# Performance work log

Hardware: AMD Instinct MI355X
Metric: run time of the kernel (lower is better)

The kernel has to match this reference:

```python
import jax, jax.numpy as jnp
import numpy as np

EMB = 128  # embsize
WORD = 128  # word_size
ITERS = 2


def _agg(embeds, neibors):
    # embeds: [B, N, D], neibors: [B, N, K] indices into node axis N (per batch)
    # mean-pool gathered neighbor embeddings -> [B, N, D]
    gathered = jax.vmap(lambda e, idx: e[idx])(embeds, neibors)  # [B, N, K, D]
    return gathered.mean(axis=2)


def setup_inputs() -> dict:
    key = jax.random.key(0)
    ks = jax.random.split(key, 9)
    B, N, K = 64, 512, 16
    word_embs = jax.random.normal(ks[0], (B, N, WORD), dtype=jnp.float32)
    lib_embs = jax.random.normal(ks[1], (B, N, WORD), dtype=jnp.float32)
    neibors = jax.random.randint(ks[2], (B, N, K), 0, N)
    neibors_lib = jax.random.randint(ks[3], (B, N, K), 0, N)
    mask = jax.random.uniform(ks[4], (B, N), dtype=jnp.float32)
    # xavier-uniform style params
    def xav(k, shape):
        bound = float(np.sqrt(6.0 / (shape[0] + shape[1])))
        return jax.random.uniform(k, shape, dtype=jnp.float32, minval=-bound, maxval=bound)
    weight = xav(ks[5], (WORD, EMB))
    weight2 = xav(ks[6], (EMB, EMB))
    enc_w1 = xav(ks[7], (WORD, EMB))
    enc_w2 = xav(ks[8], (EMB, EMB))
    return {"word_embs": word_embs, "neibors": neibors, "lib_embs": lib_embs,
            "neibors_lib": neibors_lib, "mask": mask, "weight": weight,
            "weight2": weight2, "enc_w1": enc_w1, "enc_w2": enc_w2}


def reference(word_embs, neibors, lib_embs, neibors_lib, mask, weight, weight2, enc_w1, enc_w2):
    B, N, _ = word_embs.shape
    # lib aggregation is loop-invariant (lib_embs fixed); same math as in-loop recompute
    agg_lib = jnp.einsum('bnw,we->bne', _agg(lib_embs, neibors_lib), weight)  # [B, N, EMB]
    word_proj = jnp.einsum('bnw,we->bne', word_embs, enc_w1)  # loop-invariant
    last_embed = jnp.zeros((B, N, EMB), dtype=jnp.float32)
    for _ in range(ITERS):
        agg_func = _agg(last_embed, neibors)  # [B, N, EMB]
        last_embed = jnp.tanh(word_proj + jnp.einsum('bne,ef->bnf', agg_func, enc_w2) + agg_lib)
    # masked sum over nodes, then final linear
    pooled = (last_embed * mask[:, :, None]).sum(axis=1)  # [B, EMB]
    return pooled @ weight2
```

## Files before the change

### kernel.cpp

```cpp
#include <hip/hip_runtime.h>
#include <hip/hip_bf16.h>

#define B_   64
#define N_   512
#define K_   16
#define D_   128
#define NPB  16
#define G1   ((B_*N_)/NPB)

typedef float f32x4  __attribute__((ext_vector_type(4)));
typedef short bf16x8 __attribute__((ext_vector_type(8)));

static __device__ __forceinline__ short f2bf(float x) {
    union { float f; unsigned u; } v; v.f = x;
    unsigned r = v.u + 0x7fffu + ((v.u >> 16) & 1u);
    return (short)(r >> 16);
}
static __device__ __forceinline__ float bfbits2f(unsigned hi_bits) {
    return __uint_as_float(hi_bits);
}
static __device__ __forceinline__ float bf2f(short h) {
    return __uint_as_float(((unsigned)(unsigned short)h) << 16);
}
static __device__ __forceinline__ float fast_tanh(float x) {
    float e = __expf(2.f * x);
    return 1.f - 2.f * __builtin_amdgcn_rcpf(e + 1.f);
}

__global__ __launch_bounds__(256) void prep(const float* __restrict__ lib,
                                            const float* __restrict__ enc1,
                                            const float* __restrict__ wgt,
                                            const float* __restrict__ enc2,
                                            short* __restrict__ libh,
                                            short* __restrict__ Bp1,
                                            short* __restrict__ Bp2,
                                            float* __restrict__ out) {
    const int blk = blockIdx.x;
    if (blk < 1024) {
        const size_t g = ((size_t)blk * 256 + threadIdx.x) * 16;
        short o16[16];
#pragma unroll
        for (int q = 0; q < 4; ++q) {
            float4 v = *(const float4*)&lib[g + q * 4];
            o16[q * 4 + 0] = f2bf(v.x); o16[q * 4 + 1] = f2bf(v.y);
            o16[q * 4 + 2] = f2bf(v.z); o16[q * 4 + 3] = f2bf(v.w);
        }
        *(int4*)&libh[g]     = *(int4*)o16;
        *(int4*)&libh[g + 8] = *(int4*)(o16 + 8);
        return;
    }
    int tid = (blk - 1024) * 256 + threadIdx.x;
    out[tid] = 0.f;
    short o8[8];
    if (tid < 4096) {
        int l = tid & 63, nt = (tid >> 6) & 7, ks = tid >> 9;
        int k0 = ks * 32 + (l >> 4) * 8;
        int col = nt * 16 + (l & 15);
#pragma unroll
        for (int j = 0; j < 8; ++j) {
            int r = k0 + j;
            float v = (r < 128) ? enc1[r * 128 + col] : wgt[(r - 128) * 128 + col];
            o8[j] = f2bf(v);
        }
        *(int4*)&Bp1[(size_t)tid * 8] = *(int4*)o8;
    } else if (tid < 6144) {
        int t2 = tid - 4096;
        int l = t2 & 63, nt = (t2 >> 6) & 7, ks = t2 >> 9;
        int k0 = ks * 32 + (l >> 4) * 8;
        int col = nt * 16 + (l & 15);
#pragma unroll
        for (int j = 0; j < 8; ++j) o8[j] = f2bf(enc2[(k0 + j) * 128 + col]);
        *(int4*)&Bp2[(size_t)t2 * 8] = *(int4*)o8;
    }
}

static __device__ __forceinline__ int swz_blk() {
    const int hw = blockIdx.x;
    return ((hw & 7) << 8) + (hw >> 3);
}

#define LDA1 264
__global__ __launch_bounds__(256) void gemm1(const float* __restrict__ word,
                                             const int* __restrict__ nbrL,
                                             const short* __restrict__ libh,
                                             const short* __restrict__ Bp1,
                                             short* __restrict__ baseh,
                                             short* __restrict__ t1) {
    __shared__ short sA[NPB * LDA1];
    __shared__ int sIdx[NPB * 16];
    const int tid = threadIdx.x;
    const int blk = swz_blk();
    const int b = blk >> 5;
    const int node0 = blk * NPB;

    if (tid < 64) *(int4*)&sIdx[tid * 4] = *(const int4*)&nbrL[(size_t)node0 * 16 + tid * 4];
    __syncthreads();

    const int w = tid >> 6, l = tid & 63;
    const int rh = l >> 5, c4 = l & 31;
    const short* libB = libh + (size_t)b * N_ * D_;

#pragma unroll
    for (int p = 0; p < 2; ++p) {
        const int row = 4 * w + 2 * p + rh;
        const int gid = node0 + row;
        float4 wv = *(const float4*)&word[(size_t)gid * D_ + c4 * 4];
        short4 ws; ws.x = f2bf(wv.x); ws.y = f2bf(wv.y); ws.z = f2bf(wv.z); ws.w = f2bf(wv.w);
        *(short4*)&sA[row * LDA1 + c4 * 4] = ws;
        int idxr[16];
#pragma unroll
        for (int k = 0; k < 16; ++k) idxr[k] = sIdx[row * 16 + k];
        float s0 = 0.f, s1 = 0.f, s2 = 0.f, s3 = 0.f;
#pragma unroll
        for (int k = 0; k < 16; ++k) {
            uint2 u = *(const uint2*)&libB[(size_t)idxr[k] * D_ + c4 * 4];
            s0 += bfbits2f(u.x << 16); s1 += bfbits2f(u.x & 0xffff0000u);
            s2 += bfbits2f(u.y << 16); s3 += bfbits2f(u.y & 0xffff0000u);
        }
        short4 as; as.x = f2bf(s0 * 0.0625f); as.y = f2bf(s1 * 0.0625f);
        as.z = f2bf(s2 * 0.0625f); as.w = f2bf(s3 * 0.0625f);
        *(short4*)&sA[row * LDA1 + 128 + c4 * 4] = as;
    }
    __syncthreads();

    f32x4 acc[2];
    acc[0] = (f32x4)0.f; acc[1] = (f32x4)0.f;

    const int arow = l & 15;
#pragma unroll
    for (int ks = 0; ks < 8; ++ks) {
        bf16x8 a = *(const bf16x8*)&sA[arow * LDA1 + ks * 32 + (l >> 4) * 8];
#pragma unroll
        for (int j = 0; j < 2; ++j) {
            const int nt = 2 * w + j;
            bf16x8 bb = *(const bf16x8*)&Bp1[((size_t)(ks * 8 + nt) * 64 + l) * 8];
            acc[j] = __builtin_amdgcn_mfma_f32_16x16x32_bf16(a, bb, acc[j], 0, 0, 0);
        }
    }

    const int r0 = (l >> 4) * 4;
    const int cl = l & 15;
#pragma unroll
    for (int j = 0; j < 2; ++j) {
        const int col = (2 * w + j) * 16 + cl;
#pragma unroll
        for (int r = 0; r < 4; ++r) {
            size_t o = (size_t)(node0 + r0 + r) * D_ + col;
            float v = acc[j][r];
            baseh[o] = f2bf(v);
            t1[o]    = f2bf(fast_tanh(v));
        }
    }
}

#define LDA2 136
__global__ __launch_bounds__(256) void gemm2(const short* __restrict__ t1,
                                             const int* __restrict__ nbr,
                                             const short* __restrict__ Bp2,
                                             const short* __restrict__ baseh,
                                             const float* __restrict__ mask,
                                             const float* __restrict__ w2,
                                             float* __restrict__ out) {
    __shared__ short sA[NPB * LDA2];
    __shared__ int sIdx[NPB * 16];
    __shared__ float pred[128];
    __shared__ float smask[NPB];
    const int tid = threadIdx.x;
    const int blk = swz_blk();
    const int b = blk >> 5;
    const int node0 = blk * NPB;

    if (tid < 64) *(int4*)&sIdx[tid * 4] = *(const int4*)&nbr[(size_t)node0 * 16 + tid * 4];
    if (tid >= 64 && tid < 64 + NPB) smask[tid - 64] = mask[node0 + tid - 64];
    __syncthreads();

    const int w = tid >> 6, l = tid & 63;
    const int rh = l >> 5, c4 = l & 31;
    const short* t1B = t1 + (size_t)b * N_ * D_;

#pragma unroll
    for (int p = 0; p < 2; ++p) {
        const int row = 4 * w + 2 * p + rh;
        int idxr[16];
#pragma unroll
        for (int k = 0; k < 16; ++k) idxr[k] = sIdx[row * 16 + k];
        float s0 = 0.f, s1 = 0.f, s2 = 0.f, s3 = 0.f;
#pragma unroll
        for (int k = 0; k < 16; ++k) {
            uint2 u = *(const uint2*)&t1B[(size_t)idxr[k] * D_ + c4 * 4];
            s0 += bfbits2f(u.x << 16); s1 += bfbits2f(u.x & 0xffff0000u);
            s2 += bfbits2f(u.y << 16); s3 += bfbits2f(u.y & 0xffff0000u);
        }
        short4 as; as.x = f2bf(s0 * 0.0625f); as.y = f2bf(s1 * 0.0625f);
        as.z = f2bf(s2 * 0.0625f); as.w = f2bf(s3 * 0.0625f);
        *(short4*)&sA[row * LDA2 + c4 * 4] = as;
    }
    __syncthreads();

    f32x4 acc[2];
    acc[0] = (f32x4)0.f; acc[1] = (f32x4)0.f;

    const int arow = l & 15;
#pragma unroll
    for (int ks = 0; ks < 4; ++ks) {
        bf16x8 a = *(const bf16x8*)&sA[arow * LDA2 + ks * 32 + (l >> 4) * 8];
#pragma unroll
        for (int j = 0; j < 2; ++j) {
            const int nt = 2 * w + j;
            bf16x8 bb = *(const bf16x8*)&Bp2[((size_t)(ks * 8 + nt) * 64 + l) * 8];
            acc[j] = __builtin_amdgcn_mfma_f32_16x16x32_bf16(a, bb, acc[j], 0, 0, 0);
        }
    }

    const int r0 = (l >> 4) * 4;
    const int cl = l & 15;
#pragma unroll
    for (int j = 0; j < 2; ++j) {
        const int col = (2 * w + j) * 16 + cl;
        float s = 0.f;
#pragma unroll
        for (int r = 0; r < 4; ++r) {
            size_t o = (size_t)(node0 + r0 + r) * D_ + col;
            float v = fast_tanh(bf2f(baseh[o]) + acc[j][r]);
            s += v * smask[r0 + r];
        }
        s += __shfl_xor(s, 16);
        s += __shfl_xor(s, 32);
        if (l < 16) pred[col] = s;
    }
    __syncthreads();
    if (tid < 128) {
        float a2 = 0.f;
#pragma unroll 4
        for (int f = 0; f < 128; ++f) a2 += pred[f] * w2[f * 128 + tid];
        atomicAdd(&out[b * 128 + tid], a2);
    }
}

extern "C" void kernel_launch(void* const* d_in, const int* in_sizes, int n_in,
                              void* d_out, int out_size, void* d_ws, size_t ws_size,
                              hipStream_t stream) {
    const float* word_embs   = (const float*)d_in[0];
    const int*   neibors     = (const int*)d_in[1];
    const float* lib_embs    = (const float*)d_in[2];
    const int*   neibors_lib = (const int*)d_in[3];
    const float* mask        = (const float*)d_in[4];
    const float* weight      = (const float*)d_in[5];
    const float* weight2     = (const float*)d_in[6];
    const float* enc_w1      = (const float*)d_in[7];
    const float* enc_w2      = (const float*)d_in[8];
    float* out = (float*)d_out;

    char* ws = (char*)d_ws;
    short* baseh = (short*)(ws);
    short* t1    = (short*)(ws + (1u << 23));
    short* libh  = (short*)(ws + (2u << 23));
    short* Bp1   = (short*)(ws + (3u << 23));
    short* Bp2   = (short*)(ws + (3u << 23) + 65536);

    prep<<<1056, 256, 0, stream>>>(lib_embs, enc_w1, weight, enc_w2, libh, Bp1, Bp2, out);
    gemm1<<<G1, 256, 0, stream>>>(word_embs, neibors_lib, libh, Bp1, baseh, t1);
    gemm2<<<G1, 256, 0, stream>>>(t1, neibors, Bp2, baseh, mask, weight2, out);
}
```

Measured before the change: 49.59 us.

## Switch intermediates to fp16 with packed-add gathers and folded mean scale

Converts all stored intermediates and MFMA operands from bf16 to fp16. This lets neighbor gathers accumulate with v_pk_add_f16 directly on packed data instead of unpacking to fp32. The 1/16 mean factor is folded into the weight matrices, and each thread now gathers full 16-byte rows (int4) instead of 8-byte pieces. This cuts ALU work and instruction count in the gather phase, at the cost of fp16 range and accumulation precision when summing 16 neighbors.

```diff
diff --git a/kernel.cpp b/kernel.cpp
--- a/kernel.cpp
+++ b/kernel.cpp
@@ -3,28 +3,29 @@
 
 #define B_   64
 #define N_   512
-#define K_   16
 #define D_   128
 #define NPB  16
 #define G1   ((B_*N_)/NPB)
 
 typedef float f32x4  __attribute__((ext_vector_type(4)));
-typedef short bf16x8 __attribute__((ext_vector_type(8)));
-
-static __device__ __forceinline__ short f2bf(float x) {
-    union { float f; unsigned u; } v; v.f = x;
-    unsigned r = v.u + 0x7fffu + ((v.u >> 16) & 1u);
-    return (short)(r >> 16);
-}
-static __device__ __forceinline__ float bfbits2f(unsigned hi_bits) {
-    return __uint_as_float(hi_bits);
-}
-static __device__ __forceinline__ float bf2f(short h) {
-    return __uint_as_float(((unsigned)(unsigned short)h) << 16);
+typedef _Float16 f16x8 __attribute__((ext_vector_type(8)));
+
+static __device__ __forceinline__ unsigned pkrtz(float x, float y) {
+    return __builtin_bit_cast(unsigned, __builtin_amdgcn_cvt_pkrtz(x, y));
+}
+static __device__ __forceinline__ short f2h(float x) {
+    _Float16 h = (_Float16)x;
+    return __builtin_bit_cast(short, h);
+}
+static __device__ __forceinline__ float h2f(short s) {
+    return (float)__builtin_bit_cast(_Float16, s);
 }
 static __device__ __forceinline__ float fast_tanh(float x) {
     float e = __expf(2.f * x);
     return 1.f - 2.f * __builtin_amdgcn_rcpf(e + 1.f);
+}
+static __device__ __forceinline__ void pk_add16(unsigned& acc, unsigned v) {
+    asm("v_pk_add_f16 %0, %1, %0" : "+v"(acc) : "v"(v));
 }
 
 __global__ __launch_bounds__(256) void prep(const float* __restrict__ lib,
@@ -38,15 +39,15 @@
     const int blk = blockIdx.x;
     if (blk < 1024) {
         const size_t g = ((size_t)blk * 256 + threadIdx.x) * 16;
-        short o16[16];
+        unsigned o[8];
 #pragma unroll
         for (int q = 0; q < 4; ++q) {
             float4 v = *(const float4*)&lib[g + q * 4];
-            o16[q * 4 + 0] = f2bf(v.x); o16[q * 4 + 1] = f2bf(v.y);
-            o16[q * 4 + 2] = f2bf(v.z); o16[q * 4 + 3] = f2bf(v.w);
-        }
-        *(int4*)&libh[g]     = *(int4*)o16;
-        *(int4*)&libh[g + 8] = *(int4*)(o16 + 8);
+            o[q * 2]     = pkrtz(v.x, v.y);
+            o[q * 2 + 1] = pkrtz(v.z, v.w);
+        }
+        *(int4*)&libh[g]     = *(int4*)o;
+        *(int4*)&libh[g + 8] = *(int4*)(o + 4);
         return;
     }
     int tid = (blk - 1024) * 256 + threadIdx.x;
@@ -59,8 +60,8 @@
 #pragma unroll
         for (int j = 0; j < 8; ++j) {
             int r = k0 + j;
-            float v = (r < 128) ? enc1[r * 128 + col] : wgt[(r - 128) * 128 + col];
-            o8[j] = f2bf(v);
+            float v = (r < 128) ? enc1[r * 128 + col] : wgt[(r - 128) * 128 + col] * 0.0625f;
+            o8[j] = f2h(v);
         }
         *(int4*)&Bp1[(size_t)tid * 8] = *(int4*)o8;
     } else if (tid < 6144) {
@@ -69,7 +70,7 @@
         int k0 = ks * 32 + (l >> 4) * 8;
         int col = nt * 16 + (l & 15);
 #pragma unroll
-        for (int j = 0; j < 8; ++j) o8[j] = f2bf(enc2[(k0 + j) * 128 + col]);
+        for (int j = 0; j < 8; ++j) o8[j] = f2h(enc2[(k0 + j) * 128 + col] * 0.0625f);
         *(int4*)&Bp2[(size_t)t2 * 8] = *(int4*)o8;
     }
 }
@@ -80,6 +81,8 @@
 }
 
 #define LDA1 264
+#define LDA2 136
+
 __global__ __launch_bounds__(256) void gemm1(const float* __restrict__ word,
                                              const int* __restrict__ nbrL,
                                              const short* __restrict__ libh,
@@ -96,45 +99,49 @@
     if (tid < 64) *(int4*)&sIdx[tid * 4] = *(const int4*)&nbrL[(size_t)node0 * 16 + tid * 4];
     __syncthreads();
 
+    const int row = tid >> 4;
+    const int lg  = tid & 15;
+
+    {
+        const float* wr = word + (size_t)(node0 + row) * D_ + lg * 8;
+        float4 v0 = *(const float4*)&wr[0];
+        float4 v1 = *(const float4*)&wr[4];
+        unsigned o[4] = { pkrtz(v0.x, v0.y), pkrtz(v0.z, v0.w),
+                          pkrtz(v1.x, v1.y), pkrtz(v1.z, v1.w) };
+        *(int4*)&sA[row * LDA1 + lg * 8] = *(int4*)o;
+    }
+
+    {
+        int idxr[16];
+#pragma unroll
+        for (int q = 0; q < 4; ++q) *(int4*)&idxr[q * 4] = *(const int4*)&sIdx[row * 16 + q * 4];
+        const char* libB = (const char*)libh + (size_t)b * N_ * D_ * 2 + lg * 16;
+        unsigned a0 = 0, a1 = 0, a2 = 0, a3 = 0;
+#pragma unroll
+        for (int nb = 0; nb < 16; ++nb) {
+            int4 d = *(const int4*)(libB + ((unsigned)idxr[nb] << 8));
+            pk_add16(a0, (unsigned)d.x);
+            pk_add16(a1, (unsigned)d.y);
+            pk_add16(a2, (unsigned)d.z);
+            pk_add16(a3, (unsigned)d.w);
+        }
+        unsigned o[4] = { a0, a1, a2, a3 };
+        *(int4*)&sA[row * LDA1 + 128 + lg * 8] = *(int4*)o;
+    }
+    __syncthreads();
+
     const int w = tid >> 6, l = tid & 63;
-    const int rh = l >> 5, c4 = l & 31;
-    const short* libB = libh + (size_t)b * N_ * D_;
-
-#pragma unroll
-    for (int p = 0; p < 2; ++p) {
-        const int row = 4 * w + 2 * p + rh;
-        const int gid = node0 + row;
-        float4 wv = *(const float4*)&word[(size_t)gid * D_ + c4 * 4];
-        short4 ws; ws.x = f2bf(wv.x); ws.y = f2bf(wv.y); ws.z = f2bf(wv.z); ws.w = f2bf(wv.w);
-        *(short4*)&sA[row * LDA1 + c4 * 4] = ws;
-        int idxr[16];
-#pragma unroll
-        for (int k = 0; k < 16; ++k) idxr[k] = sIdx[row * 16 + k];
-        float s0 = 0.f, s1 = 0.f, s2 = 0.f, s3 = 0.f;
-#pragma unroll
-        for (int k = 0; k < 16; ++k) {
-            uint2 u = *(const uint2*)&libB[(size_t)idxr[k] * D_ + c4 * 4];
-            s0 += bfbits2f(u.x << 16); s1 += bfbits2f(u.x & 0xffff0000u);
-            s2 += bfbits2f(u.y << 16); s3 += bfbits2f(u.y & 0xffff0000u);
-        }
-        short4 as; as.x = f2bf(s0 * 0.0625f); as.y = f2bf(s1 * 0.0625f);
-        as.z = f2bf(s2 * 0.0625f); as.w = f2bf(s3 * 0.0625f);
-        *(short4*)&sA[row * LDA1 + 128 + c4 * 4] = as;
-    }
-    __syncthreads();
-
     f32x4 acc[2];
     acc[0] = (f32x4)0.f; acc[1] = (f32x4)0.f;
-
     const int arow = l & 15;
 #pragma unroll
     for (int ks = 0; ks < 8; ++ks) {
-        bf16x8 a = *(const bf16x8*)&sA[arow * LDA1 + ks * 32 + (l >> 4) * 8];
+        f16x8 a = *(const f16x8*)&sA[arow * LDA1 + ks * 32 + (l >> 4) * 8];
 #pragma unroll
         for (int j = 0; j < 2; ++j) {
             const int nt = 2 * w + j;
-            bf16x8 bb = *(const bf16x8*)&Bp1[((size_t)(ks * 8 + nt) * 64 + l) * 8];
-            acc[j] = __builtin_amdgcn_mfma_f32_16x16x32_bf16(a, bb, acc[j], 0, 0, 0);
+            f16x8 bb = *(const f16x8*)&Bp1[((size_t)(ks * 8 + nt) * 64 + l) * 8];
+            acc[j] = __builtin_amdgcn_mfma_f32_16x16x32_f16(a, bb, acc[j], 0, 0, 0);
         }
     }
 
@@ -147,13 +154,12 @@
         for (int r = 0; r < 4; ++r) {
             size_t o = (size_t)(node0 + r0 + r) * D_ + col;
             float v = acc[j][r];
-            baseh[o] = f2bf(v);
-            t1[o]    = f2bf(fast_tanh(v));
-        }
-    }
-}
-
-#define LDA2 136
+            baseh[o] = f2h(v);
+            t1[o]    = f2h(fast_tanh(v));
+        }
+    }
+}
+
 __global__ __launch_bounds__(256) void gemm2(const short* __restrict__ t1,
                                              const int* __restrict__ nbr,
                                              const short* __restrict__ Bp2,
@@ -174,41 +180,39 @@
     if (tid >= 64 && tid < 64 + NPB) smask[tid - 64] = mask[node0 + tid - 64];
     __syncthreads();
 
+    const int row = tid >> 4;
+    const int lg  = tid & 15;
+    {
+        int idxr[16];
+#pragma unroll
+        for (int q = 0; q < 4; ++q) *(int4*)&idxr[q * 4] = *(const int4*)&sIdx[row * 16 + q * 4];
+        const char* tB = (const char*)t1 + (size_t)b * N_ * D_ * 2 + lg * 16;
+        unsigned a0 = 0, a1 = 0, a2 = 0, a3 = 0;
+#pragma unroll
+        for (int nb = 0; nb < 16; ++nb) {
+            int4 d = *(const int4*)(tB + ((unsigned)idxr[nb] << 8));
+            pk_add16(a0, (unsigned)d.x);
+            pk_add16(a1, (unsigned)d.y);
+            pk_add16(a2, (unsigned)d.z);
+            pk_add16(a3, (unsigned)d.w);
+        }
+        unsigned o[4] = { a0, a1, a2, a3 };
+        *(int4*)&sA[row * LDA2 + lg * 8] = *(int4*)o;
+    }
+    __syncthreads();
+
     const int w = tid >> 6, l = tid & 63;
-    const int rh = l >> 5, c4 = l & 31;
-    const short* t1B = t1 + (size_t)b * N_ * D_;
-
-#pragma unroll
-    for (int p = 0; p < 2; ++p) {
-        const int row = 4 * w + 2 * p + rh;
-        int idxr[16];
-#pragma unroll
-        for (int k = 0; k < 16; ++k) idxr[k] = sIdx[row * 16 + k];
-        float s0 = 0.f, s1 = 0.f, s2 = 0.f, s3 = 0.f;
-#pragma unroll
-        for (int k = 0; k < 16; ++k) {
-            uint2 u = *(const uint2*)&t1B[(size_t)idxr[k] * D_ + c4 * 4];
-            s0 += bfbits2f(u.x << 16); s1 += bfbits2f(u.x & 0xffff0000u);
-            s2 += bfbits2f(u.y << 16); s3 += bfbits2f(u.y & 0xffff0000u);
-        }
-        short4 as; as.x = f2bf(s0 * 0.0625f); as.y = f2bf(s1 * 0.0625f);
-        as.z = f2bf(s2 * 0.0625f); as.w = f2bf(s3 * 0.0625f);
-        *(short4*)&sA[row * LDA2 + c4 * 4] = as;
-    }
-    __syncthreads();
-
     f32x4 acc[2];
     acc[0] = (f32x4)0.f; acc[1] = (f32x4)0.f;
-
     const int arow = l & 15;
 #pragma unroll
     for (int ks = 0; ks < 4; ++ks) {
-        bf16x8 a = *(const bf16x8*)&sA[arow * LDA2 + ks * 32 + (l >> 4) * 8];
+        f16x8 a = *(const f16x8*)&sA[arow * LDA2 + ks * 32 + (l >> 4) * 8];
 #pragma unroll
         for (int j = 0; j < 2; ++j) {
             const int nt = 2 * w + j;
-            bf16x8 bb = *(const bf16x8*)&Bp2[((size_t)(ks * 8 + nt) * 64 + l) * 8];
-            acc[j] = __builtin_amdgcn_mfma_f32_16x16x32_bf16(a, bb, acc[j], 0, 0, 0);
+            f16x8 bb = *(const f16x8*)&Bp2[((size_t)(ks * 8 + nt) * 64 + l) * 8];
+            acc[j] = __builtin_amdgcn_mfma_f32_16x16x32_f16(a, bb, acc[j], 0, 0, 0);
         }
     }
 
@@ -221,7 +225,7 @@
 #pragma unroll
         for (int r = 0; r < 4; ++r) {
             size_t o = (size_t)(node0 + r0 + r) * D_ + col;
-            float v = fast_tanh(bf2f(baseh[o]) + acc[j][r]);
+            float v = fast_tanh(h2f(baseh[o]) + acc[j][r]);
             s += v * smask[r0 + r];
         }
         s += __shfl_xor(s, 16);
```

New measurement: 48.29 us, median of 2. 2.6% less time.
